# Performance work log

Hardware: AMD Instinct MI355X
Metric: run time of the kernel (lower is better)

## Reference

```python
import jax, jax.numpy as jnp
import numpy as np
import math

B, T, N_CTX, H = 4, 512, 2048, 1024
NUM_HEADS, NUM_INSTRUMENTS, MAX_BARS = 16, 16, 8
HEAD_DIM = H // NUM_HEADS


def setup_inputs() -> dict:
    key = jax.random.key(0)
    ks = jax.random.split(key, 16)
    s = 1.0 / math.sqrt(H)
    return {
        "query": jax.random.normal(ks[0], (B, T, H), jnp.float32),
        "context": jax.random.normal(ks[1], (B, N_CTX, H), jnp.float32),
        "instrument_ids": jax.random.randint(ks[2], (B, N_CTX), 0, NUM_INSTRUMENTS),
        "current_instrument_id": 3,
        "bar_offsets": jax.random.randint(ks[3], (B, N_CTX), 0, MAX_BARS),
        "Wq": jax.random.normal(ks[4], (H, H), jnp.float32) * s,
        "bq": jnp.zeros((H,), jnp.float32),
        "Wk": jax.random.normal(ks[5], (H, H), jnp.float32) * s,
        "bk": jnp.zeros((H,), jnp.float32),
        "Wv": jax.random.normal(ks[6], (H, H), jnp.float32) * s,
        "bv": jnp.zeros((H,), jnp.float32),
        "Wo": jax.random.normal(ks[7], (H, H), jnp.float32) * s,
        "bo": jnp.zeros((H,), jnp.float32),
        "inst_emb": jax.random.normal(ks[8], (NUM_INSTRUMENTS, H), jnp.float32),
        "bar_emb": jax.random.normal(ks[9], (MAX_BARS, H), jnp.float32),
    }


def reference(query, context, instrument_ids, current_instrument_id, bar_offsets,
              Wq, bq, Wk, bk, Wv, bv, Wo, bo, inst_emb, bar_emb):
    # current_instrument_id: python int -> broadcast to (B,)
    cur = jnp.full((B,), current_instrument_id, dtype=jnp.int64 if instrument_ids.dtype == jnp.int64 else jnp.int32)
    # add embeddings to query and context
    q = query + inst_emb[cur][:, None, :]                              # (B,T,H)
    ctx = context + inst_emb[instrument_ids] + bar_emb[jnp.clip(bar_offsets, 0, MAX_BARS - 1)]  # (B,N,H)
    # projections (torch Linear: x @ W.T + b)
    Q = (q @ Wq.T + bq).reshape(B, T, NUM_HEADS, HEAD_DIM).transpose(0, 2, 1, 3)      # (B,h,T,d)
    K = (ctx @ Wk.T + bk).reshape(B, N_CTX, NUM_HEADS, HEAD_DIM).transpose(0, 2, 1, 3)  # (B,h,N,d)
    V = (ctx @ Wv.T + bv).reshape(B, N_CTX, NUM_HEADS, HEAD_DIM).transpose(0, 2, 1, 3)  # (B,h,N,d)
    scores = jnp.einsum('bhtd,bhnd->bhtn', Q, K) / math.sqrt(HEAD_DIM)  # (B,h,T,N)
    # attend only to keys whose instrument differs from the current one
    keep = (instrument_ids != cur[:, None])[:, None, None, :]           # (B,1,1,N)
    scores = jnp.where(keep, scores, jnp.float32(-1e9))
    probs = jax.nn.softmax(scores, axis=-1)
    out = jnp.einsum('bhtn,bhnd->bhtd', probs, V).transpose(0, 2, 1, 3).reshape(B, T, H)
    return out @ Wo.T + bo
```

## Files before the change

kernel.cpp:

```cpp
#include <hip/hip_runtime.h>

#define H 1024
#define B_ 4
#define T_ 512
#define NCTX 2048
#define NH 16
#define HD 64

typedef __attribute__((ext_vector_type(8))) short bf16x8;
typedef __attribute__((ext_vector_type(4))) float f32x4;
typedef __attribute__((ext_vector_type(4))) short s16x4;

__device__ __forceinline__ ushort f2b(float f) {
  union { float f; unsigned u; } v; v.f = f;
  unsigned u = v.u;
  unsigned r = (u + 0x7FFFu + ((u >> 16) & 1u)) >> 16;
  return (ushort)r;
}

__device__ __forceinline__ void gld16(const void* g, void* l) {
  __builtin_amdgcn_global_load_lds((const __attribute__((address_space(1))) unsigned int*)g,
                                   (__attribute__((address_space(3))) unsigned int*)l, 16, 0, 0);
}


__global__ void cvt4_kernel(const float* __restrict__ s0, const float* __restrict__ s1,
                            const float* __restrict__ s2, const float* __restrict__ s3,
                            ushort* __restrict__ d0, ushort* __restrict__ d1,
                            ushort* __restrict__ d2, ushort* __restrict__ d3) {
  int blk = blockIdx.x;
  int which = blk >> 10;
  int i = (blk & 1023) * 256 + threadIdx.x;
  const float* s = which == 0 ? s0 : which == 1 ? s1 : which == 2 ? s2 : s3;
  ushort* d = which == 0 ? d0 : which == 1 ? d1 : which == 2 ? d2 : d3;
  float4 v = ((const float4*)s)[i];
  s16x4 o;
  o[0] = (short)f2b(v.x); o[1] = (short)f2b(v.y);
  o[2] = (short)f2b(v.z); o[3] = (short)f2b(v.w);
  ((s16x4*)d)[i] = o;
}

__global__ void prep_q_kernel(const float* __restrict__ q, const float* __restrict__ iemb,
                              const int* __restrict__ curp, ushort* __restrict__ out) {
  int cur = curp[0];
  int i = blockIdx.x * blockDim.x + threadIdx.x;
  int c4 = i & 255;
  float4 v = ((const float4*)q)[i];
  float4 e = ((const float4*)(iemb + (size_t)cur * H))[c4];
  s16x4 o;
  o[0] = (short)f2b(v.x + e.x); o[1] = (short)f2b(v.y + e.y);
  o[2] = (short)f2b(v.z + e.z); o[3] = (short)f2b(v.w + e.w);
  ((s16x4*)out)[i] = o;
}

__global__ void prep_ctx_kernel(const float* __restrict__ ctx, const float* __restrict__ iemb,
                                const float* __restrict__ bemb, const int* __restrict__ ids,
                                const int* __restrict__ bars, ushort* __restrict__ out) {
  int i = blockIdx.x * blockDim.x + threadIdx.x;
  int row = i >> 8;
  int c4 = i & 255;
  int id = ids[row];
  int bar = bars[row];
  bar = bar < 0 ? 0 : (bar > 7 ? 7 : bar);
  float4 v = ((const float4*)ctx)[i];
  float4 e = ((const float4*)(iemb + (size_t)id * H))[c4];
  float4 g = ((const float4*)(bemb + (size_t)bar * H))[c4];
  s16x4 o;
  o[0] = (short)f2b(v.x + e.x + g.x); o[1] = (short)f2b(v.y + e.y + g.y);
  o[2] = (short)f2b(v.z + e.z + g.z); o[3] = (short)f2b(v.w + e.w + g.w);
  ((s16x4*)out)[i] = o;
}


__global__ __launch_bounds__(256) void proj_k(const ushort* __restrict__ Aq,
                                              const ushort* __restrict__ Actx,
                                              const ushort* __restrict__ WQ,
                                              const ushort* __restrict__ WK,
                                              const ushort* __restrict__ WV,
                                              const float* __restrict__ bQ,
                                              const float* __restrict__ bK,
                                              const float* __restrict__ bV,
                                              ushort* __restrict__ Qout,
                                              ushort* __restrict__ Kout,
                                              ushort* __restrict__ VTout) {
  const int id = blockIdx.x;
  const ushort* A;
  const ushort* W;
  const float* bias;
  int row0, col0, mode;
  ushort* Cout;
  if (id < 1024) {
    int xcd = id & 7, rest = id >> 3;
    int bx = rest & 15, by = (rest >> 4) * 8 + xcd;
    A = Actx; row0 = by * 128;
    if (bx < 8) { W = WK; bias = bK; col0 = bx * 128; mode = 0; Cout = Kout; }
    else        { W = WV; bias = bV; col0 = (bx - 8) * 128; mode = 1; Cout = VTout; }
  } else {
    int q = id - 1024;
    A = Aq; row0 = (q >> 3) * 128; col0 = (q & 7) * 128;
    W = WQ; bias = bQ; mode = 2; Cout = Qout;
  }

  __shared__ ushort As[128 * 32];
  __shared__ ushort Bs[128 * 32];
  const int tid = threadIdx.x;
  const int lane = tid & 63;
  const int wv = tid >> 6;
  const int wr = wv >> 1, wc = wv & 1;
  const int lo = lane & 15, hi = lane >> 4;

  f32x4 acc[4][4];
#pragma unroll
  for (int m = 0; m < 4; m++)
#pragma unroll
    for (int n = 0; n < 4; n++) acc[m][n] = (f32x4){0.f, 0.f, 0.f, 0.f};

  for (int kt = 0; kt < H; kt += 32) {
#pragma unroll
    for (int c = 0; c < 2; c++) {
      int ia = wv * 128 + c * 64 + lane;
      int r = ia >> 2, s = ia & 3;
      gld16(A + (size_t)(row0 + r) * H + kt + s * 8, (char*)As + (wv * 128 + c * 64) * 16);
      gld16(W + (size_t)(col0 + r) * H + kt + s * 8, (char*)Bs + (wv * 128 + c * 64) * 16);
    }
    __syncthreads();
    bf16x8 af[4], bfr[4];
#pragma unroll
    for (int m = 0; m < 4; m++) af[m] = *(const bf16x8*)(As + (wr * 64 + m * 16 + lo) * 32 + hi * 8);
#pragma unroll
    for (int n = 0; n < 4; n++) bfr[n] = *(const bf16x8*)(Bs + (wc * 64 + n * 16 + lo) * 32 + hi * 8);
#pragma unroll
    for (int m = 0; m < 4; m++)
#pragma unroll
      for (int n = 0; n < 4; n++)
        acc[m][n] = __builtin_amdgcn_mfma_f32_16x16x32_bf16(af[m], bfr[n], acc[m][n], 0, 0, 0);
    __syncthreads();
  }

#pragma unroll
  for (int m = 0; m < 4; m++) {
    int gr0 = row0 + wr * 64 + m * 16 + hi * 4;
#pragma unroll
    for (int n = 0; n < 4; n++) {
      int gc = col0 + wc * 64 + n * 16 + lo;
      float bv = bias[gc];
      if (mode == 0) {
#pragma unroll
        for (int r = 0; r < 4; r++)
          Cout[(size_t)(gr0 + r) * H + gc] = f2b(acc[m][n][r] + bv);
      } else if (mode == 1) {
        int bb = gr0 >> 11, n0 = gr0 & 2047;
        s16x4 o;
#pragma unroll
        for (int r = 0; r < 4; r++) o[r] = (short)f2b(acc[m][n][r] + bv);
        *(s16x4*)(Cout + (size_t)bb * (H * NCTX) + (size_t)gc * NCTX + n0) = o;
      } else {
#pragma unroll
        for (int r = 0; r < 4; r++)
          Cout[(size_t)(gr0 + r) * H + gc] = f2b((acc[m][n][r] + bv) * 0.125f);
      }
    }
  }
}


__global__ __launch_bounds__(256) void gemm_o(const ushort* __restrict__ A,
                                              const ushort* __restrict__ W,
                                              const float* __restrict__ bias,
                                              float* __restrict__ Cout) {
  __shared__ ushort As[128 * 32];
  __shared__ ushort Bs[128 * 32];
  const int tid = threadIdx.x;
  const int lane = tid & 63;
  const int wv = tid >> 6;
  const int wr = wv >> 1, wc = wv & 1;
  const int lo = lane & 15, hi = lane >> 4;
  const int row0 = blockIdx.y * 128, col0 = blockIdx.x * 128;

  f32x4 acc[4][4];
#pragma unroll
  for (int m = 0; m < 4; m++)
#pragma unroll
    for (int n = 0; n < 4; n++) acc[m][n] = (f32x4){0.f, 0.f, 0.f, 0.f};

  for (int kt = 0; kt < H; kt += 32) {
#pragma unroll
    for (int c = 0; c < 2; c++) {
      int ia = wv * 128 + c * 64 + lane;
      int r = ia >> 2, s = ia & 3;
      gld16(A + (size_t)(row0 + r) * H + kt + s * 8, (char*)As + (wv * 128 + c * 64) * 16);
      gld16(W + (size_t)(col0 + r) * H + kt + s * 8, (char*)Bs + (wv * 128 + c * 64) * 16);
    }
    __syncthreads();
    bf16x8 af[4], bfr[4];
#pragma unroll
    for (int m = 0; m < 4; m++) af[m] = *(const bf16x8*)(As + (wr * 64 + m * 16 + lo) * 32 + hi * 8);
#pragma unroll
    for (int n = 0; n < 4; n++) bfr[n] = *(const bf16x8*)(Bs + (wc * 64 + n * 16 + lo) * 32 + hi * 8);
#pragma unroll
    for (int m = 0; m < 4; m++)
#pragma unroll
      for (int n = 0; n < 4; n++)
        acc[m][n] = __builtin_amdgcn_mfma_f32_16x16x32_bf16(af[m], bfr[n], acc[m][n], 0, 0, 0);
    __syncthreads();
  }

#pragma unroll
  for (int m = 0; m < 4; m++) {
    int gr0 = row0 + wr * 64 + m * 16 + hi * 4;
#pragma unroll
    for (int n = 0; n < 4; n++) {
      int gc = col0 + wc * 64 + n * 16 + lo;
      float bv = bias[gc];
#pragma unroll
      for (int r = 0; r < 4; r++)
        Cout[(size_t)(gr0 + r) * H + gc] = acc[m][n][r] + bv;
    }
  }
}


#define NSPLIT 2
#define KVLEN (NCTX / NSPLIT)
#define NT_KV (KVLEN / 64)

__global__ __launch_bounds__(256) void attn_k(const ushort* __restrict__ Q,
                                              const ushort* __restrict__ K,
                                              const ushort* __restrict__ VT,
                                              const int* __restrict__ ids,
                                              const int* __restrict__ curp,
                                              float* __restrict__ OPf,
                                              float* __restrict__ mlf) {
  __shared__ ushort Ks[2][64 * 64];
  __shared__ ushort Vs[2][64 * 64];
  __shared__ ushort Ps[4][16 * 64];
  const int blk = (blockIdx.x & 7) * 128 + (blockIdx.x >> 3);
  const int qt = blk & 7;
  const int h = (blk >> 3) & 15;
  const int b = (blk >> 7) & 3;
  const int p = blk >> 9;
  const int cur = curp[0];
  const int tid = threadIdx.x, lane = tid & 63, w = tid >> 6;
  const int lo = lane & 15, hi = lane >> 4;
  const int swz = (lo & 7) << 4;
  const int kvbase = p * KVLEN;

  const ushort* Qp = Q + ((size_t)(b * T_ + qt * 64 + w * 16 + lo)) * H + h * HD;
  bf16x8 qf0 = *(const bf16x8*)(Qp + hi * 8);
  bf16x8 qf1 = *(const bf16x8*)(Qp + 32 + hi * 8);

  f32x4 oacc[4];
#pragma unroll
  for (int d = 0; d < 4; d++) oacc[d] = (f32x4){0.f, 0.f, 0.f, 0.f};
  float mrow = -1e30f, lrow = 0.f;

  const int* idb = ids + b * NCTX;
  const ushort* Kbase = K + ((size_t)(b * NCTX)) * H + h * HD;
  const ushort* Vbase = VT + (size_t)b * (H * NCTX) + (size_t)(h * HD) * NCTX;

  bf16x8 kr[2], vr[2];
#pragma unroll
  for (int i = 0; i < 2; i++) {
    int seg = tid + i * 256;
    int r = seg >> 3, s = seg & 7;
    kr[i] = *(const bf16x8*)(Kbase + (size_t)(kvbase + r) * H + s * 8);
    vr[i] = *(const bf16x8*)(Vbase + (size_t)r * NCTX + kvbase + s * 8);
  }
#pragma unroll
  for (int i = 0; i < 2; i++) {
    int seg = tid + i * 256;
    int r = seg >> 3, s = seg & 7;
    int wb = (r * 128 + s * 16) ^ ((r & 7) << 4);
    *(bf16x8*)((char*)Ks[0] + wb) = kr[i];
    *(bf16x8*)((char*)Vs[0] + wb) = vr[i];
  }
  __syncthreads();

  int curbuf = 0;
  for (int t = 0; t < NT_KV; t++) {
    int kvt = kvbase + t * 64;
    if (t < NT_KV - 1) {
#pragma unroll
      for (int i = 0; i < 2; i++) {
        int seg = tid + i * 256;
        int r = seg >> 3, s = seg & 7;
        kr[i] = *(const bf16x8*)(Kbase + (size_t)(kvt + 64 + r) * H + s * 8);
        vr[i] = *(const bf16x8*)(Vbase + (size_t)r * NCTX + kvt + 64 + s * 8);
      }
    }

    f32x4 sc[4];
#pragma unroll
    for (int nt = 0; nt < 4; nt++) {
      bf16x8 kf0 = *(const bf16x8*)((char*)Ks[curbuf] + ((((nt * 16 + lo) * 128) + hi * 16) ^ swz));
      bf16x8 kf1 = *(const bf16x8*)((char*)Ks[curbuf] + ((((nt * 16 + lo) * 128) + 64 + hi * 16) ^ swz));
      f32x4 z = (f32x4){0.f, 0.f, 0.f, 0.f};
      z = __builtin_amdgcn_mfma_f32_16x16x32_bf16(kf0, qf0, z, 0, 0, 0);
      sc[nt] = __builtin_amdgcn_mfma_f32_16x16x32_bf16(kf1, qf1, z, 0, 0, 0);
    }

    float pv[4][4];
#pragma unroll
    for (int nt = 0; nt < 4; nt++) {
      int4 iv = *(const int4*)(idb + kvt + nt * 16 + hi * 4);
      pv[nt][0] = (iv.x != cur) ? sc[nt][0] : -1e30f;
      pv[nt][1] = (iv.y != cur) ? sc[nt][1] : -1e30f;
      pv[nt][2] = (iv.z != cur) ? sc[nt][2] : -1e30f;
      pv[nt][3] = (iv.w != cur) ? sc[nt][3] : -1e30f;
    }

    float x = fmaxf(fmaxf(fmaxf(pv[0][0], pv[0][1]), fmaxf(pv[0][2], pv[0][3])),
                    fmaxf(fmaxf(pv[1][0], pv[1][1]), fmaxf(pv[1][2], pv[1][3])));
    x = fmaxf(x, fmaxf(fmaxf(fmaxf(pv[2][0], pv[2][1]), fmaxf(pv[2][2], pv[2][3])),
                       fmaxf(fmaxf(pv[3][0], pv[3][1]), fmaxf(pv[3][2], pv[3][3]))));
    x = fmaxf(x, __shfl_xor(x, 16));
    x = fmaxf(x, __shfl_xor(x, 32));
    bool defer = __all((x <= mrow + 8.0f) && (mrow > -1e29f));
    float mn, scal = 1.f;
    if (defer) {
      mn = mrow;
    } else {
      mn = fmaxf(mrow, x);
      scal = __expf(mrow - mn);
      mrow = mn;
    }
    float rs = 0.f;
#pragma unroll
    for (int nt = 0; nt < 4; nt++)
#pragma unroll
      for (int r = 0; r < 4; r++) {
        float e = __expf(pv[nt][r] - mn);
        pv[nt][r] = e;
        rs += e;
      }
    rs += __shfl_xor(rs, 16);
    rs += __shfl_xor(rs, 32);
    if (defer) {
      lrow += rs;
    } else {
      lrow = lrow * scal + rs;
      float sq0 = __shfl(scal, hi * 4 + 0);
      float sq1 = __shfl(scal, hi * 4 + 1);
      float sq2 = __shfl(scal, hi * 4 + 2);
      float sq3 = __shfl(scal, hi * 4 + 3);
#pragma unroll
      for (int d = 0; d < 4; d++) {
        oacc[d][0] *= sq0; oacc[d][1] *= sq1; oacc[d][2] *= sq2; oacc[d][3] *= sq3;
      }
    }

#pragma unroll
    for (int nt = 0; nt < 4; nt++) {
      s16x4 pw;
#pragma unroll
      for (int r = 0; r < 4; r++) pw[r] = (short)f2b(pv[nt][r]);
      *(s16x4*)((char*)Ps[w] + ((lo * 128 + (nt * 16 + hi * 4) * 2) ^ swz)) = pw;
    }

#pragma unroll
    for (int ks = 0; ks < 2; ks++) {
      bf16x8 pa = *(const bf16x8*)((char*)Ps[w] + ((lo * 128 + (ks * 64 + hi * 16)) ^ swz));
#pragma unroll
      for (int d = 0; d < 4; d++) {
        bf16x8 vf = *(const bf16x8*)((char*)Vs[curbuf] + (((d * 16 + lo) * 128 + ks * 64 + hi * 16) ^ swz));
        oacc[d] = __builtin_amdgcn_mfma_f32_16x16x32_bf16(pa, vf, oacc[d], 0, 0, 0);
      }
    }

    if (t < NT_KV - 1) {
#pragma unroll
      for (int i = 0; i < 2; i++) {
        int seg = tid + i * 256;
        int r = seg >> 3, s = seg & 7;
        int wb = (r * 128 + s * 16) ^ ((r & 7) << 4);
        *(bf16x8*)((char*)Ks[curbuf ^ 1] + wb) = kr[i];
        *(bf16x8*)((char*)Vs[curbuf ^ 1] + wb) = vr[i];
      }
    }
    __syncthreads();
    curbuf ^= 1;
  }

  int row0 = b * 512 + qt * 64 + w * 16 + hi * 4;
#pragma unroll
  for (int d = 0; d < 4; d++) {
#pragma unroll
    for (int r = 0; r < 4; r++)
      OPf[((size_t)p * 2048 + row0 + r) * 1024 + h * 64 + d * 16 + lo] = oacc[d][r];
  }
  if (hi == 0) {
    int qrow = b * 512 + qt * 64 + w * 16 + lo;
    mlf[(((size_t)p * 2048 + qrow) * 16 + h) * 2] = mrow;
    mlf[(((size_t)p * 2048 + qrow) * 16 + h) * 2 + 1] = lrow;
  }
}

__global__ void attn_combine(const float* __restrict__ OPf, const float* __restrict__ mlf,
                             ushort* __restrict__ O) {
  int idx = blockIdx.x * 256 + threadIdx.x;
  int btr = idx >> 8;
  int c4 = idx & 255;
  int h = c4 >> 4;
  float m0 = mlf[((size_t)btr * 16 + h) * 2];
  float l0 = mlf[((size_t)btr * 16 + h) * 2 + 1];
  float m1 = mlf[(((size_t)2048 + btr) * 16 + h) * 2];
  float l1 = mlf[(((size_t)2048 + btr) * 16 + h) * 2 + 1];
  float M = fmaxf(m0, m1);
  float a0 = __expf(m0 - M), a1 = __expf(m1 - M);
  float inv = 1.0f / (a0 * l0 + a1 * l1);
  float4 o0 = ((const float4*)OPf)[idx];
  float4 o1 = ((const float4*)OPf)[(size_t)524288 + idx];
  s16x4 r;
  r[0] = (short)f2b((a0 * o0.x + a1 * o1.x) * inv);
  r[1] = (short)f2b((a0 * o0.y + a1 * o1.y) * inv);
  r[2] = (short)f2b((a0 * o0.z + a1 * o1.z) * inv);
  r[3] = (short)f2b((a0 * o0.w + a1 * o1.w) * inv);
  ((s16x4*)O)[idx] = r;
}


extern "C" void kernel_launch(void* const* d_in, const int* in_sizes, int n_in,
                              void* d_out, int out_size, void* d_ws, size_t ws_size,
                              hipStream_t stream) {
  const float* query = (const float*)d_in[0];
  const float* context = (const float*)d_in[1];
  const int* ids = (const int*)d_in[2];
  const int* curp = (const int*)d_in[3];
  const int* bars = (const int*)d_in[4];
  const float* Wq = (const float*)d_in[5];
  const float* bq = (const float*)d_in[6];
  const float* Wk = (const float*)d_in[7];
  const float* bk = (const float*)d_in[8];
  const float* Wv = (const float*)d_in[9];
  const float* bv = (const float*)d_in[10];
  const float* Wo = (const float*)d_in[11];
  const float* bo = (const float*)d_in[12];
  const float* iemb = (const float*)d_in[13];
  const float* bemb = (const float*)d_in[14];
  float* out = (float*)d_out;

  ushort* ws = (ushort*)d_ws;
  ushort* Wqb = ws;
  ushort* Wkb = Wqb + (1u << 20);
  ushort* Wvb = Wkb + (1u << 20);
  ushort* Wob = Wvb + (1u << 20);
  ushort* qin = Wob + (1u << 20);
  ushort* ctxb = qin + (2u << 20);
  ushort* Qb = ctxb + (8u << 20);
  ushort* Kb = Qb + (2u << 20);
  ushort* VTb = Kb + (8u << 20);
  ushort* AOb = VTb + (8u << 20);

  float* OPf = (float*)ctxb;
  float* mlf = (float*)qin;

  cvt4_kernel<<<4096, 256, 0, stream>>>(Wq, Wk, Wv, Wo, Wqb, Wkb, Wvb, Wob);
  prep_q_kernel<<<2048, 256, 0, stream>>>(query, iemb, curp, qin);
  prep_ctx_kernel<<<8192, 256, 0, stream>>>(context, iemb, bemb, ids, bars, ctxb);

  proj_k<<<1152, 256, 0, stream>>>(qin, ctxb, Wqb, Wkb, Wvb, bq, bk, bv, Qb, Kb, VTb);

  attn_k<<<1024, 256, 0, stream>>>(Qb, Kb, VTb, ids, curp, OPf, mlf);
  attn_combine<<<2048, 256, 0, stream>>>(OPf, mlf, AOb);

  gemm_o<<<dim3(8, 16), 256, 0, stream>>>(AOb, Wob, bo, out);
}
```

Baseline: 166.8 us.

## Double-buffer LDS tiles in projection GEMMs and fuse prep kernels into one launch

The projection and output GEMMs now use two LDS buffers, issuing the async global-to-LDS loads for the next K tile before computing on the current one. This removes one barrier per iteration and lets the loads overlap the MFMA work. The three elementwise prep/convert kernels are merged into a single launch to cut launch overhead and inter-kernel gaps. Doubling LDS per block may reduce occupancy. Correctness depends on the global_load_lds completion being covered by the single barrier at the end of each iteration.

```diff
diff --git a/kernel.cpp b/kernel.cpp
--- a/kernel.cpp
+++ b/kernel.cpp
@@ -24,51 +24,52 @@
 }
 
 
-__global__ void cvt4_kernel(const float* __restrict__ s0, const float* __restrict__ s1,
-                            const float* __restrict__ s2, const float* __restrict__ s3,
-                            ushort* __restrict__ d0, ushort* __restrict__ d1,
-                            ushort* __restrict__ d2, ushort* __restrict__ d3) {
+__global__ void prep_all(const float* __restrict__ query, const float* __restrict__ ctx,
+                         const int* __restrict__ ids, const int* __restrict__ curp,
+                         const int* __restrict__ bars,
+                         const float* __restrict__ iemb, const float* __restrict__ bemb,
+                         const float* __restrict__ Wq, const float* __restrict__ Wk,
+                         const float* __restrict__ Wv, const float* __restrict__ Wo,
+                         ushort* __restrict__ qin, ushort* __restrict__ ctxb,
+                         ushort* __restrict__ Wqb, ushort* __restrict__ Wkb,
+                         ushort* __restrict__ Wvb, ushort* __restrict__ Wob) {
   int blk = blockIdx.x;
-  int which = blk >> 10;
-  int i = (blk & 1023) * 256 + threadIdx.x;
-  const float* s = which == 0 ? s0 : which == 1 ? s1 : which == 2 ? s2 : s3;
-  ushort* d = which == 0 ? d0 : which == 1 ? d1 : which == 2 ? d2 : d3;
-  float4 v = ((const float4*)s)[i];
-  s16x4 o;
-  o[0] = (short)f2b(v.x); o[1] = (short)f2b(v.y);
-  o[2] = (short)f2b(v.z); o[3] = (short)f2b(v.w);
-  ((s16x4*)d)[i] = o;
-}
-
-__global__ void prep_q_kernel(const float* __restrict__ q, const float* __restrict__ iemb,
-                              const int* __restrict__ curp, ushort* __restrict__ out) {
-  int cur = curp[0];
-  int i = blockIdx.x * blockDim.x + threadIdx.x;
-  int c4 = i & 255;
-  float4 v = ((const float4*)q)[i];
-  float4 e = ((const float4*)(iemb + (size_t)cur * H))[c4];
-  s16x4 o;
-  o[0] = (short)f2b(v.x + e.x); o[1] = (short)f2b(v.y + e.y);
-  o[2] = (short)f2b(v.z + e.z); o[3] = (short)f2b(v.w + e.w);
-  ((s16x4*)out)[i] = o;
-}
-
-__global__ void prep_ctx_kernel(const float* __restrict__ ctx, const float* __restrict__ iemb,
-                                const float* __restrict__ bemb, const int* __restrict__ ids,
-                                const int* __restrict__ bars, ushort* __restrict__ out) {
-  int i = blockIdx.x * blockDim.x + threadIdx.x;
-  int row = i >> 8;
-  int c4 = i & 255;
-  int id = ids[row];
-  int bar = bars[row];
-  bar = bar < 0 ? 0 : (bar > 7 ? 7 : bar);
-  float4 v = ((const float4*)ctx)[i];
-  float4 e = ((const float4*)(iemb + (size_t)id * H))[c4];
-  float4 g = ((const float4*)(bemb + (size_t)bar * H))[c4];
-  s16x4 o;
-  o[0] = (short)f2b(v.x + e.x + g.x); o[1] = (short)f2b(v.y + e.y + g.y);
-  o[2] = (short)f2b(v.z + e.z + g.z); o[3] = (short)f2b(v.w + e.w + g.w);
-  ((s16x4*)out)[i] = o;
+  if (blk < 8192) {
+    int i = blk * 256 + threadIdx.x;
+    int row = i >> 8;
+    int c4 = i & 255;
+    int id = ids[row];
+    int bar = bars[row];
+    bar = bar < 0 ? 0 : (bar > 7 ? 7 : bar);
+    float4 v = ((const float4*)ctx)[i];
+    float4 e = ((const float4*)(iemb + (size_t)id * H))[c4];
+    float4 g = ((const float4*)(bemb + (size_t)bar * H))[c4];
+    s16x4 o;
+    o[0] = (short)f2b(v.x + e.x + g.x); o[1] = (short)f2b(v.y + e.y + g.y);
+    o[2] = (short)f2b(v.z + e.z + g.z); o[3] = (short)f2b(v.w + e.w + g.w);
+    ((s16x4*)ctxb)[i] = o;
+  } else if (blk < 10240) {
+    int cur = curp[0];
+    int i = (blk - 8192) * 256 + threadIdx.x;
+    int c4 = i & 255;
+    float4 v = ((const float4*)query)[i];
+    float4 e = ((const float4*)(iemb + (size_t)cur * H))[c4];
+    s16x4 o;
+    o[0] = (short)f2b(v.x + e.x); o[1] = (short)f2b(v.y + e.y);
+    o[2] = (short)f2b(v.z + e.z); o[3] = (short)f2b(v.w + e.w);
+    ((s16x4*)qin)[i] = o;
+  } else {
+    int b2 = blk - 10240;
+    int which = b2 >> 10;
+    int i = (b2 & 1023) * 256 + threadIdx.x;
+    const float* s = which == 0 ? Wq : which == 1 ? Wk : which == 2 ? Wv : Wo;
+    ushort* d = which == 0 ? Wqb : which == 1 ? Wkb : which == 2 ? Wvb : Wob;
+    float4 v = ((const float4*)s)[i];
+    s16x4 o;
+    o[0] = (short)f2b(v.x); o[1] = (short)f2b(v.y);
+    o[2] = (short)f2b(v.z); o[3] = (short)f2b(v.w);
+    ((s16x4*)d)[i] = o;
+  }
 }
 
 
@@ -101,8 +102,8 @@
     W = WQ; bias = bQ; mode = 2; Cout = Qout;
   }
 
-  __shared__ ushort As[128 * 32];
-  __shared__ ushort Bs[128 * 32];
+  __shared__ ushort As[2][128 * 32];
+  __shared__ ushort Bs[2][128 * 32];
   const int tid = threadIdx.x;
   const int lane = tid & 63;
   const int wv = tid >> 6;
@@ -115,26 +116,40 @@
 #pragma unroll
     for (int n = 0; n < 4; n++) acc[m][n] = (f32x4){0.f, 0.f, 0.f, 0.f};
 
-  for (int kt = 0; kt < H; kt += 32) {
-#pragma unroll
-    for (int c = 0; c < 2; c++) {
-      int ia = wv * 128 + c * 64 + lane;
-      int r = ia >> 2, s = ia & 3;
-      gld16(A + (size_t)(row0 + r) * H + kt + s * 8, (char*)As + (wv * 128 + c * 64) * 16);
-      gld16(W + (size_t)(col0 + r) * H + kt + s * 8, (char*)Bs + (wv * 128 + c * 64) * 16);
-    }
-    __syncthreads();
+#pragma unroll
+  for (int c = 0; c < 2; c++) {
+    int ia = wv * 128 + c * 64 + lane;
+    int r = ia >> 2, s = ia & 3;
+    gld16(A + (size_t)(row0 + r) * H + s * 8, (char*)As[0] + (wv * 128 + c * 64) * 16);
+    gld16(W + (size_t)(col0 + r) * H + s * 8, (char*)Bs[0] + (wv * 128 + c * 64) * 16);
+  }
+  __syncthreads();
+
+  int cur = 0;
+  for (int kt = 0; kt < 32; kt++) {
+    if (kt < 31) {
+#pragma unroll
+      for (int c = 0; c < 2; c++) {
+        int ia = wv * 128 + c * 64 + lane;
+        int r = ia >> 2, s = ia & 3;
+        gld16(A + (size_t)(row0 + r) * H + (kt + 1) * 32 + s * 8,
+              (char*)As[cur ^ 1] + (wv * 128 + c * 64) * 16);
+        gld16(W + (size_t)(col0 + r) * H + (kt + 1) * 32 + s * 8,
+              (char*)Bs[cur ^ 1] + (wv * 128 + c * 64) * 16);
+      }
+    }
     bf16x8 af[4], bfr[4];
 #pragma unroll
-    for (int m = 0; m < 4; m++) af[m] = *(const bf16x8*)(As + (wr * 64 + m * 16 + lo) * 32 + hi * 8);
-#pragma unroll
-    for (int n = 0; n < 4; n++) bfr[n] = *(const bf16x8*)(Bs + (wc * 64 + n * 16 + lo) * 32 + hi * 8);
+    for (int m = 0; m < 4; m++) af[m] = *(const bf16x8*)(As[cur] + (wr * 64 + m * 16 + lo) * 32 + hi * 8);
+#pragma unroll
+    for (int n = 0; n < 4; n++) bfr[n] = *(const bf16x8*)(Bs[cur] + (wc * 64 + n * 16 + lo) * 32 + hi * 8);
 #pragma unroll
     for (int m = 0; m < 4; m++)
 #pragma unroll
       for (int n = 0; n < 4; n++)
         acc[m][n] = __builtin_amdgcn_mfma_f32_16x16x32_bf16(af[m], bfr[n], acc[m][n], 0, 0, 0);
     __syncthreads();
+    cur ^= 1;
   }
 
 #pragma unroll
@@ -168,8 +183,8 @@
                                               const ushort* __restrict__ W,
                                               const float* __restrict__ bias,
                                               float* __restrict__ Cout) {
-  __shared__ ushort As[128 * 32];
-  __shared__ ushort Bs[128 * 32];
+  __shared__ ushort As[2][128 * 32];
+  __shared__ ushort Bs[2][128 * 32];
   const int tid = threadIdx.x;
   const int lane = tid & 63;
   const int wv = tid >> 6;
@@ -183,26 +198,40 @@
 #pragma unroll
     for (int n = 0; n < 4; n++) acc[m][n] = (f32x4){0.f, 0.f, 0.f, 0.f};
 
-  for (int kt = 0; kt < H; kt += 32) {
-#pragma unroll
-    for (int c = 0; c < 2; c++) {
-      int ia = wv * 128 + c * 64 + lane;
-      int r = ia >> 2, s = ia & 3;
-      gld16(A + (size_t)(row0 + r) * H + kt + s * 8, (char*)As + (wv * 128 + c * 64) * 16);
-      gld16(W + (size_t)(col0 + r) * H + kt + s * 8, (char*)Bs + (wv * 128 + c * 64) * 16);
-    }
-    __syncthreads();
+#pragma unroll
+  for (int c = 0; c < 2; c++) {
+    int ia = wv * 128 + c * 64 + lane;
+    int r = ia >> 2, s = ia & 3;
+    gld16(A + (size_t)(row0 + r) * H + s * 8, (char*)As[0] + (wv * 128 + c * 64) * 16);
+    gld16(W + (size_t)(col0 + r) * H + s * 8, (char*)Bs[0] + (wv * 128 + c * 64) * 16);
+  }
+  __syncthreads();
+
+  int cur = 0;
+  for (int kt = 0; kt < 32; kt++) {
+    if (kt < 31) {
+#pragma unroll
+      for (int c = 0; c < 2; c++) {
+        int ia = wv * 128 + c * 64 + lane;
+        int r = ia >> 2, s = ia & 3;
+        gld16(A + (size_t)(row0 + r) * H + (kt + 1) * 32 + s * 8,
+              (char*)As[cur ^ 1] + (wv * 128 + c * 64) * 16);
+        gld16(W + (size_t)(col0 + r) * H + (kt + 1) * 32 + s * 8,
+              (char*)Bs[cur ^ 1] + (wv * 128 + c * 64) * 16);
+      }
+    }
     bf16x8 af[4], bfr[4];
 #pragma unroll
-    for (int m = 0; m < 4; m++) af[m] = *(const bf16x8*)(As + (wr * 64 + m * 16 + lo) * 32 + hi * 8);
-#pragma unroll
-    for (int n = 0; n < 4; n++) bfr[n] = *(const bf16x8*)(Bs + (wc * 64 + n * 16 + lo) * 32 + hi * 8);
+    for (int m = 0; m < 4; m++) af[m] = *(const bf16x8*)(As[cur] + (wr * 64 + m * 16 + lo) * 32 + hi * 8);
+#pragma unroll
+    for (int n = 0; n < 4; n++) bfr[n] = *(const bf16x8*)(Bs[cur] + (wc * 64 + n * 16 + lo) * 32 + hi * 8);
 #pragma unroll
     for (int m = 0; m < 4; m++)
 #pragma unroll
       for (int n = 0; n < 4; n++)
         acc[m][n] = __builtin_amdgcn_mfma_f32_16x16x32_bf16(af[m], bfr[n], acc[m][n], 0, 0, 0);
     __syncthreads();
+    cur ^= 1;
   }
 
 #pragma unroll
@@ -454,9 +483,8 @@
   float* OPf = (float*)ctxb;
   float* mlf = (float*)qin;
 
-  cvt4_kernel<<<4096, 256, 0, stream>>>(Wq, Wk, Wv, Wo, Wqb, Wkb, Wvb, Wob);
-  prep_q_kernel<<<2048, 256, 0, stream>>>(query, iemb, curp, qin);
-  prep_ctx_kernel<<<8192, 256, 0, stream>>>(context, iemb, bemb, ids, bars, ctxb);
+  prep_all<<<14336, 256, 0, stream>>>(query, context, ids, curp, bars, iemb, bemb,
+                                      Wq, Wk, Wv, Wo, qin, ctxb, Wqb, Wkb, Wvb, Wob);
 
   proj_k<<<1152, 256, 0, stream>>>(qin, ctxb, Wqb, Wkb, Wvb, bq, bk, bv, Qb, Kb, VTb);
 
```

After: 160.3 us. 1.04x faster.
